# Performance work log

Hardware: AMD Instinct MI355X
Metric: run time of the kernel (lower is better)

The kernel has to match this reference:

```python
import jax, jax.numpy as jnp
import numpy as np

VOCAB = 30000  # opts.numofingr
EPS = 1e-12


def setup_inputs() -> dict:
    key = jax.random.key(0)
    ks = jax.random.split(key, 8)
    B, L = 4096, 20
    ingrs = jax.random.randint(ks[0], (B, L), 0, VOCAB, dtype=jnp.int32)
    lengths = jax.random.randint(ks[1], (B,), 0, 21, dtype=jnp.int32)
    # MLP params: Linear(VOCAB,512) -> ReLU -> Linear(512,1024) -> ReLU -> Linear(1024,2047)
    # Stored so that one-hot @ W1 == W1[ingr]; i.e. W1 has shape [VOCAB, 512].
    W1 = jax.random.normal(ks[2], (VOCAB, 512), dtype=jnp.float32) * (1.0 / np.sqrt(VOCAB))
    b1 = jax.random.normal(ks[3], (512,), dtype=jnp.float32) * 0.01
    W2 = jax.random.normal(ks[4], (512, 1024), dtype=jnp.float32) * (1.0 / np.sqrt(512))
    b2 = jax.random.normal(ks[5], (1024,), dtype=jnp.float32) * 0.01
    W3 = jax.random.normal(ks[6], (1024, 2047), dtype=jnp.float32) * (1.0 / np.sqrt(1024))
    b3 = jax.random.normal(ks[7], (2047,), dtype=jnp.float32) * 0.01
    return {"ingrs": ingrs, "lengths": lengths,
            "W1": W1, "b1": b1, "W2": W2, "b2": b2, "W3": W3, "b3": b3}


def reference(ingrs, lengths, W1, b1, W2, b2, W3, b3):
    # One-hot x MLP first layer == embedding row gather: [B, L, 512]
    h1 = jax.nn.relu(W1[ingrs] + b1)
    h2 = jax.nn.relu(jnp.einsum('blh,hk->blk', h1, W2) + b2)   # [B, L, 1024]
    emb = jnp.einsum('blk,ko->blo', h2, W3) + b3               # [B, L, 2047]
    # L2-normalize each ingredient embedding (torch norm(p=2, dim=1) on [1,2047])
    nrm = jnp.sqrt(jnp.sum(emb * emb, axis=-1, keepdims=True))
    emb = emb / jnp.maximum(nrm, EPS)
    # Masked sum over valid ingredients (ingr_ln truncation in the source)
    L = ingrs.shape[1]
    mask = (jnp.arange(L)[None, :] < lengths[:, None]).astype(emb.dtype)  # [B, L]
    return jnp.einsum('blo,bl->bo', emb, mask)                 # [B, 2047]
```

## Files before the change

kernel.cpp:

```cpp
#include <hip/hip_runtime.h>

#define VOCAB 30000
#define MPAD  30080
#define MT_PAD 240

typedef __attribute__((ext_vector_type(8))) short bf16x8;
typedef __attribute__((ext_vector_type(4))) float f32x4;

__device__ __forceinline__ unsigned short f2bf(float f) {
    unsigned int u = __builtin_bit_cast(unsigned int, f);
    u += 0x7fffu + ((u >> 16) & 1u);
    return (unsigned short)(u >> 16);
}
__device__ __forceinline__ float bf2f(unsigned int h) {
    unsigned int u = h << 16;
    return __builtin_bit_cast(float, u);
}

__device__ __forceinline__ void async16(const void* g, void* l) {
    __builtin_amdgcn_global_load_lds(
        (__attribute__((address_space(1))) void*)g,
        (__attribute__((address_space(3))) void*)l, 16, 0, 0);
}

__global__ void k_mark(const int* __restrict__ ingrs, const int* __restrict__ lengths,
                       int* __restrict__ flags, int* __restrict__ cnt)
{
    const int i = blockIdx.x * 256 + threadIdx.x;
    if (i == 0) *cnt = 0;
    if (i >= 4096 * 20) return;
    const int b = i / 20;
    const int l = i - b * 20;
    if (l < lengths[b]) flags[ingrs[i]] = 1;
}

__global__ void k_assign(const int* __restrict__ flags, int* __restrict__ remap,
                         int* __restrict__ cnt)
{
    const int i = blockIdx.x * 256 + threadIdx.x;
    if (i < VOCAB && flags[i] == 1) remap[i] = atomicAdd(cnt, 1);
}


__device__ __forceinline__ void transpose_body(
    const float* __restrict__ in, unsigned short* __restrict__ out,
    int K, int Nin, int n0, int k0, int tid, float (*t)[65])
{
#pragma unroll
    for (int p = 0; p < 16; ++p) {
        const int lin = p * 256 + tid;
        const int kk = lin >> 6, nn = lin & 63;
        const int n = n0 + nn;
        t[kk][nn] = (n < Nin) ? in[(size_t)(k0 + kk) * Nin + n] : 0.f;
    }
    __syncthreads();
#pragma unroll
    for (int p = 0; p < 16; ++p) {
        const int lin = p * 256 + tid;
        const int nn = lin >> 6, kk = lin & 63;
        out[(size_t)(n0 + nn) * K + k0 + kk] = f2bf(t[kk][nn]);
    }
}

__device__ __forceinline__ void gemm_body(
    unsigned short* smem,
    const unsigned short* __restrict__ A, const unsigned short* __restrict__ BT,
    const float* __restrict__ bias, int bias_n, unsigned short* __restrict__ C,
    int K, int N, int relu, int mc, int id, int nt_shift)
{
    const int w  = id >> 3;
    const int n_tile = w & ((1 << nt_shift) - 1);
    const int m_tile = (id & 7) + ((w >> nt_shift) << 3);
    const int m0 = m_tile * 128;
    if (m0 >= mc) return;
    const int n0 = n_tile * 128;

    unsigned short* As = smem;
    unsigned short* Bs = smem + 8192;

    const int tid  = threadIdx.x;
    const int lane = tid & 63;
    const int wid  = tid >> 6;
    const int wr   = wid >> 1;
    const int wc   = wid & 1;
    const int q  = lane >> 4;
    const int ml = lane & 15;

    f32x4 acc[4][4];
    const f32x4 zero = {0.f, 0.f, 0.f, 0.f};
#pragma unroll
    for (int i = 0; i < 4; ++i)
#pragma unroll
        for (int j = 0; j < 4; ++j) acc[i][j] = zero;

    const int rg = lane >> 3;
    const int kc = (lane & 7) ^ rg;
    const unsigned short* pA = A  + (size_t)(m0 + wid * 32 + rg) * K + kc * 8;
    const unsigned short* pB = BT + (size_t)(n0 + wid * 32 + rg) * K + kc * 8;
    unsigned short* lA = &As[wid * 4 * 512 + lane * 8];
    unsigned short* lB = &Bs[wid * 4 * 512 + lane * 8];

    const int swz0 = (q ^ (ml & 7)) * 8;

    for (int k0 = 0; k0 < K; k0 += 64) {
#pragma unroll
        for (int gg = 0; gg < 4; ++gg) {
            async16(pA + (size_t)gg * 8 * K, lA + gg * 512);
            async16(pB + (size_t)gg * 8 * K, lB + gg * 512);
        }
        pA += 64; pB += 64;
        __syncthreads();

        bf16x8 af[4], bfr[4];
#pragma unroll
        for (int t = 0; t < 4; ++t) {
            af[t]  = *(const bf16x8*)&As[(wr * 64 + t * 16 + ml) * 64 + swz0];
            bfr[t] = *(const bf16x8*)&Bs[(wc * 64 + t * 16 + ml) * 64 + swz0];
        }
#pragma unroll
        for (int i = 0; i < 4; ++i)
#pragma unroll
            for (int j = 0; j < 4; ++j)
                acc[i][j] = __builtin_amdgcn_mfma_f32_16x16x32_bf16(
                    af[i], bfr[j], acc[i][j], 0, 0, 0);
#pragma unroll
        for (int t = 0; t < 4; ++t) {
            af[t]  = *(const bf16x8*)&As[(wr * 64 + t * 16 + ml) * 64 + (swz0 ^ 32)];
            bfr[t] = *(const bf16x8*)&Bs[(wc * 64 + t * 16 + ml) * 64 + (swz0 ^ 32)];
        }
#pragma unroll
        for (int i = 0; i < 4; ++i)
#pragma unroll
            for (int j = 0; j < 4; ++j)
                acc[i][j] = __builtin_amdgcn_mfma_f32_16x16x32_bf16(
                    af[i], bfr[j], acc[i][j], 0, 0, 0);

        __syncthreads();
    }

#pragma unroll
    for (int i = 0; i < 4; ++i) {
#pragma unroll
        for (int j = 0; j < 4; ++j) {
#pragma unroll
            for (int r = 0; r < 4; ++r) {
                const int rl = wr * 64 + i * 16 + q * 4 + r;
                const int cl = wc * 64 + j * 16 + ml;
                float v = acc[i][j][r];
                const int col = n0 + cl;
                v += (col < bias_n) ? bias[col] : 0.f;
                if (relu) v = fmaxf(v, 0.f);
                smem[rl * 136 + cl] = f2bf(v);
            }
        }
    }
    __syncthreads();
#pragma unroll
    for (int p = 0; p < 8; ++p) {
        const int rr = p * 16 + (tid >> 4);
        const int cc = tid & 15;
        const uint4 val = *(const uint4*)&smem[rr * 136 + cc * 8];
        *(uint4*)&C[(size_t)(m0 + rr) * N + n0 + cc * 8] = val;
    }
}

__global__ __launch_bounds__(256)
void k_prep(const float* __restrict__ W1, const float* __restrict__ b1,
            const int* __restrict__ flags, const int* __restrict__ remap,
            unsigned short* __restrict__ A1,
            const float* __restrict__ W2, unsigned short* __restrict__ W2T)
{
    __shared__ float t[64][65];
    const int bid = blockIdx.x;
    const int tid = threadIdx.x;

    if (bid < 15000) {
        const int id = bid * 2 + (tid >> 7);
        if (flags[id] != 1) return;
        const int row = remap[id];
        const int k4  = (tid & 127) * 4;
        const float4 w  = *(const float4*)(W1 + (size_t)id * 512 + k4);
        const float4 bb = *(const float4*)(b1 + k4);
        unsigned short o[4];
        o[0] = f2bf(fmaxf(w.x + bb.x, 0.f));
        o[1] = f2bf(fmaxf(w.y + bb.y, 0.f));
        o[2] = f2bf(fmaxf(w.z + bb.z, 0.f));
        o[3] = f2bf(fmaxf(w.w + bb.w, 0.f));
        *(uint2*)(A1 + (size_t)row * 512 + k4) = *(const uint2*)o;
    } else {
        const int local = bid - 15000;
        transpose_body(W2, W2T, 512, 1024, (local & 15) * 64, (local >> 4) * 64, tid, t);
    }
}

__global__ __launch_bounds__(256)
void k_gemm1(const unsigned short* __restrict__ A1, const unsigned short* __restrict__ W2T,
             const float* __restrict__ b2, unsigned short* __restrict__ H2,
             const int* __restrict__ cnt,
             const float* __restrict__ W3, unsigned short* __restrict__ W3T,
             const int* __restrict__ ingrs, const int* __restrict__ lengths,
             const int* __restrict__ remap, int* __restrict__ slots)
{
    __shared__ __align__(16) unsigned short smem[128 * 136];
    const int bid = blockIdx.x;
    if (bid < MT_PAD * 8) {
        const int mc = (*cnt + 127) & ~127;
        gemm_body(smem, A1, W2T, b2, 1024, H2, 512, 1024, 1, mc, bid, 3);
    } else if (bid < MT_PAD * 8 + 512) {
        const int local = bid - MT_PAD * 8;
        transpose_body(W3, W3T, 1024, 2047, (local & 31) * 64, (local >> 5) * 64,
                       threadIdx.x, (float(*)[65])smem);
    } else {
        const int i = (bid - (MT_PAD * 8 + 512)) * 256 + threadIdx.x;
        if (i < 4096 * 20) {
            const int b = i / 20;
            const int l = i - b * 20;
            if (l < lengths[b]) slots[i] = remap[ingrs[i]];
        }
    }
}

#define G2_NK 16
#define G2_K  1024
#define G2_N  2048
#define G2_MT 120

#define MF(a, b, c) __builtin_amdgcn_mfma_f32_16x16x32_bf16(a, b, c, 0, 0, 0)

__global__ __launch_bounds__(512, 2)
void k_gemm2(const unsigned short* __restrict__ A, const unsigned short* __restrict__ BT,
             const float* __restrict__ bias, unsigned short* __restrict__ C,
             const int* __restrict__ cnt)
{
    __shared__ __align__(16) unsigned short lds[65536];

    const int id = blockIdx.x;
    const int w  = id >> 3;
    const int n_tile = w & 7;
    const int m_tile = (id & 7) + ((w >> 3) << 3);
    const int m0 = m_tile * 256;
    const int mc = (*cnt + 255) & ~255;
    if (m0 >= mc) return;
    const int n0 = n_tile * 256;

    const int tid  = threadIdx.x;
    const int lane = tid & 63;
    const int w0   = tid >> 6;
    const int wr   = w0 >> 2;
    const int wc   = w0 & 3;
    const int q    = lane >> 4;
    const int ml   = lane & 15;
    const int m7   = ml & 7;

    f32x4 acc[8][4];
    const f32x4 zero = {0.f, 0.f, 0.f, 0.f};
#pragma unroll
    for (int i = 0; i < 8; ++i)
#pragma unroll
        for (int j = 0; j < 4; ++j) acc[i][j] = zero;

    const int rg = lane >> 3;
    const int kc = (lane & 7) ^ rg;
    const unsigned short* pA0 = A  + (size_t)(m0 + w0 * 32 + rg) * G2_K + kc * 8;
    const unsigned short* pB0 = BT + (size_t)(n0 + w0 * 32 + rg) * G2_K + kc * 8;
    const int dstoff = w0 * 2048 + lane * 8;

#define G2_STAGE(BUF, KT) do {                                             \
        const unsigned short* _sa = pA0 + (size_t)(KT) * 64;               \
        const unsigned short* _sb = pB0 + (size_t)(KT) * 64;               \
        unsigned short* _da = &lds[(BUF) * 16384 + dstoff];                \
        unsigned short* _db = &lds[32768 + (BUF) * 16384 + dstoff];        \
        _Pragma("unroll")                                                  \
        for (int g = 0; g < 4; ++g) {                                      \
            async16(_sa + (size_t)g * 8 * G2_K, _da + g * 512);            \
            async16(_sb + (size_t)g * 8 * G2_K, _db + g * 512);            \
        }                                                                  \
    } while (0)

#define LDA(I, S) (*(const bf16x8*)&lds[cb + ((wr * 128 + (I) * 16 + ml) * 64) + ((((S) * 4 + q) ^ m7) * 8)])
#define LDB(J, S) (*(const bf16x8*)&lds[32768 + cb + ((wc * 64 + (J) * 16 + ml) * 64) + ((((S) * 4 + q) ^ m7) * 8)])

#define G2_PHASE(I0) do {                                                  \
        bf16x8 a00 = LDA(I0, 0), a01 = LDA(I0, 1);                         \
        bf16x8 a10 = LDA(I0 + 1, 0), a11 = LDA(I0 + 1, 1);                 \
        __builtin_amdgcn_s_barrier();                                      \
        asm volatile("s_waitcnt lgkmcnt(0)" ::: "memory");                 \
        __builtin_amdgcn_sched_barrier(0);                                 \
        __builtin_amdgcn_s_setprio(1);                                     \
        _Pragma("unroll")                                                  \
        for (int j = 0; j < 4; ++j) acc[I0][j]     = MF(a00, bfr[0][j], acc[I0][j]);     \
        _Pragma("unroll")                                                  \
        for (int j = 0; j < 4; ++j) acc[I0 + 1][j] = MF(a10, bfr[0][j], acc[I0 + 1][j]); \
        _Pragma("unroll")                                                  \
        for (int j = 0; j < 4; ++j) acc[I0][j]     = MF(a01, bfr[1][j], acc[I0][j]);     \
        _Pragma("unroll")                                                  \
        for (int j = 0; j < 4; ++j) acc[I0 + 1][j] = MF(a11, bfr[1][j], acc[I0 + 1][j]); \
        __builtin_amdgcn_s_setprio(0);                                     \
        __builtin_amdgcn_s_barrier();                                      \
    } while (0)

    G2_STAGE(0, 0);
    G2_STAGE(1, 1);
    asm volatile("s_waitcnt vmcnt(8)" ::: "memory");
    __builtin_amdgcn_s_barrier();

    for (int t = 0; t < G2_NK; ++t) {
        const int cb = (t & 1) * 16384;

        bf16x8 bfr[2][4];
#pragma unroll
        for (int s = 0; s < 2; ++s)
#pragma unroll
            for (int j = 0; j < 4; ++j) bfr[s][j] = LDB(j, s);

        G2_PHASE(0);
        G2_PHASE(2);
        G2_PHASE(4);
        G2_PHASE(6);

        if (t + 2 < G2_NK) {
            G2_STAGE(t & 1, t + 2);
            asm volatile("s_waitcnt vmcnt(8)" ::: "memory");
        } else {
            asm volatile("s_waitcnt vmcnt(0)" ::: "memory");
        }
        __builtin_amdgcn_s_barrier();
    }

#undef G2_PHASE
#undef LDA
#undef LDB
#undef G2_STAGE

    float bv[4];
#pragma unroll
    for (int j = 0; j < 4; ++j) {
        const int col = n0 + wc * 64 + j * 16 + ml;
        bv[j] = (col < 2047) ? bias[col] : 0.f;
    }
    for (int h = 0; h < 2; ++h) {
        if (wr == h) {
#pragma unroll
            for (int i = 0; i < 8; ++i)
#pragma unroll
                for (int j = 0; j < 4; ++j)
#pragma unroll
                    for (int r = 0; r < 4; ++r) {
                        const float v = acc[i][j][r] + bv[j];
                        lds[(i * 16 + q * 4 + r) * 280 + wc * 64 + j * 16 + ml] = f2bf(v);
                    }
        }
        __syncthreads();
#pragma unroll
        for (int p = 0; p < 8; ++p) {
            const int row  = p * 16 + (tid >> 5);
            const int c8   = (tid & 31) * 8;
            const int grow = m0 + h * 128 + row;
            if (grow < MPAD) {
                *(uint4*)&C[(size_t)grow * G2_N + n0 + c8] =
                    *(const uint4*)&lds[row * 280 + c8];
            }
        }
        __syncthreads();
    }
}

__global__ __launch_bounds__(64)
void k_gather(const int* __restrict__ lengths, const int* __restrict__ slots,
              const unsigned short* __restrict__ Table, float* __restrict__ out)
{
    const int b    = blockIdx.x;
    const int lane = threadIdx.x;

    float acc[32];
#pragma unroll
    for (int j = 0; j < 32; ++j) acc[j] = 0.f;

    const int len = lengths[b];
    if (len > 0) {
        uint4 u[4];
        {
            const int slot = slots[b * 20];
            const uint4* rp = (const uint4*)(Table + (size_t)slot * 2048);
#pragma unroll
            for (int c = 0; c < 4; ++c) u[c] = rp[c * 64 + lane];
        }
        for (int l = 0; l < len; ++l) {
            uint4 cu[4];
#pragma unroll
            for (int c = 0; c < 4; ++c) cu[c] = u[c];
            if (l + 1 < len) {
                const int ns = slots[b * 20 + l + 1];
                const uint4* rp = (const uint4*)(Table + (size_t)ns * 2048);
#pragma unroll
                for (int c = 0; c < 4; ++c) u[c] = rp[c * 64 + lane];
            }
            float v[32];
#pragma unroll
            for (int c = 0; c < 4; ++c) {
                v[c*8+0] = bf2f(cu[c].x & 0xffffu); v[c*8+1] = bf2f(cu[c].x >> 16);
                v[c*8+2] = bf2f(cu[c].y & 0xffffu); v[c*8+3] = bf2f(cu[c].y >> 16);
                v[c*8+4] = bf2f(cu[c].z & 0xffffu); v[c*8+5] = bf2f(cu[c].z >> 16);
                v[c*8+6] = bf2f(cu[c].w & 0xffffu); v[c*8+7] = bf2f(cu[c].w >> 16);
            }
            float s = 0.f;
#pragma unroll
            for (int j = 0; j < 32; ++j) s += v[j] * v[j];
#pragma unroll
            for (int off = 1; off < 64; off <<= 1) s += __shfl_xor(s, off, 64);
            const float invn = 1.0f / fmaxf(sqrtf(s), 1e-12f);
#pragma unroll
            for (int j = 0; j < 32; ++j) acc[j] += v[j] * invn;
        }
    }

    const size_t base = (size_t)b * 2047;
#pragma unroll
    for (int c = 0; c < 4; ++c) {
        const int col = (c * 64 + lane) * 8;
#pragma unroll
        for (int j = 0; j < 8; ++j)
            if (col + j < 2047) out[base + col + j] = acc[c * 8 + j];
    }
}


extern "C" void kernel_launch(void* const* d_in, const int* in_sizes, int n_in,
                              void* d_out, int out_size, void* d_ws, size_t ws_size,
                              hipStream_t stream)
{
    const int*   ingrs   = (const int*)d_in[0];
    const int*   lengths = (const int*)d_in[1];
    const float* W1 = (const float*)d_in[2];
    const float* b1 = (const float*)d_in[3];
    const float* W2 = (const float*)d_in[4];
    const float* b2 = (const float*)d_in[5];
    const float* W3 = (const float*)d_in[6];
    const float* b3 = (const float*)d_in[7];
    float* out = (float*)d_out;

    char* ws = (char*)d_ws;
    unsigned short* A1    = (unsigned short*)(ws);
    unsigned short* H2    = (unsigned short*)(ws + 30801920);
    unsigned short* Table = (unsigned short*)(ws + 92405760);
    unsigned short* W2T   = (unsigned short*)(ws + 215613440);
    unsigned short* W3T   = (unsigned short*)(ws + 216662016);
    int*            flags = (int*)(ws + 220856320);
    int*            remap = (int*)(ws + 220976320);
    int*            cnt   = (int*)(ws + 221096320);
    int*            slots = (int*)(ws + 221216448);

    k_mark  <<<(4096 * 20 + 255) / 256, 256, 0, stream>>>(ingrs, lengths, flags, cnt);
    k_assign<<<(VOCAB + 255) / 256, 256, 0, stream>>>(flags, remap, cnt);
    k_prep<<<15128, 256, 0, stream>>>(W1, b1, flags, remap, A1, W2, W2T);
    k_gemm1<<<MT_PAD * 8 + 512 + 320, 256, 0, stream>>>(
        A1, W2T, b2, H2, cnt, W3, W3T, ingrs, lengths, remap, slots);
    k_gemm2<<<G2_MT * 8, 512, 0, stream>>>(H2, W3T, b3, Table, cnt);

    k_gather<<<4096, 64, 0, stream>>>(lengths, slots, Table, out);
}
```

Baseline: 320.5 us.

## Split GEMM tile loads into half-tile units interleaved with MFMA phases

The GEMM main loop is restructured so global-to-LDS async loads are issued as half-tile units (top/bottom 128 rows of A and B), and those units are interleaved across four MFMA phases instead of being issued all at once after compute. The phases now work on 4x4 MFMA blocks per K-slice rather than 2 rows across both slices. The aim is to spread memory traffic through the compute and keep the prefetch pipeline fuller. This adds finer-grained buffer-hazard reasoning: the next-buffer loads for the second half are issued while the current buffer is still being read, which risks races if the barrier ordering is wrong.

```diff
diff --git a/kernel.cpp b/kernel.cpp
--- a/kernel.cpp
+++ b/kernel.cpp
@@ -261,76 +261,91 @@
 
     const int rg = lane >> 3;
     const int kc = (lane & 7) ^ rg;
-    const unsigned short* pA0 = A  + (size_t)(m0 + w0 * 32 + rg) * G2_K + kc * 8;
-    const unsigned short* pB0 = BT + (size_t)(n0 + w0 * 32 + rg) * G2_K + kc * 8;
-    const int dstoff = w0 * 2048 + lane * 8;
-
-#define G2_STAGE(BUF, KT) do {                                             \
-        const unsigned short* _sa = pA0 + (size_t)(KT) * 64;               \
-        const unsigned short* _sb = pB0 + (size_t)(KT) * 64;               \
-        unsigned short* _da = &lds[(BUF) * 16384 + dstoff];                \
-        unsigned short* _db = &lds[32768 + (BUF) * 16384 + dstoff];        \
-        _Pragma("unroll")                                                  \
-        for (int g = 0; g < 4; ++g) {                                      \
-            async16(_sa + (size_t)g * 8 * G2_K, _da + g * 512);            \
-            async16(_sb + (size_t)g * 8 * G2_K, _db + g * 512);            \
-        }                                                                  \
+    const unsigned short* gA = A  + (size_t)(m0 + w0 * 16 + rg) * G2_K + kc * 8;
+    const unsigned short* gB = BT + (size_t)(n0 + w0 * 16 + rg) * G2_K + kc * 8;
+    const int dst0 = (w0 * 16) * 64 + lane * 8;
+
+#define G2_U(AB, H, B_, T) do {                                                \
+        const unsigned short* _s = ((AB) ? gB : gA)                            \
+            + (size_t)((H) * 128) * G2_K + (size_t)(T) * 64;                   \
+        unsigned short* _d = &lds[(AB) * 32768 + (B_) * 16384                  \
+            + ((H) * 128) * 64 + dst0];                                        \
+        async16(_s, _d);                                                       \
+        async16(_s + (size_t)8 * G2_K, _d + 8 * 64);                           \
     } while (0)
 
 #define LDA(I, S) (*(const bf16x8*)&lds[cb + ((wr * 128 + (I) * 16 + ml) * 64) + ((((S) * 4 + q) ^ m7) * 8)])
 #define LDB(J, S) (*(const bf16x8*)&lds[32768 + cb + ((wc * 64 + (J) * 16 + ml) * 64) + ((((S) * 4 + q) ^ m7) * 8)])
 
-#define G2_PHASE(I0) do {                                                  \
-        bf16x8 a00 = LDA(I0, 0), a01 = LDA(I0, 1);                         \
-        bf16x8 a10 = LDA(I0 + 1, 0), a11 = LDA(I0 + 1, 1);                 \
-        __builtin_amdgcn_s_barrier();                                      \
-        asm volatile("s_waitcnt lgkmcnt(0)" ::: "memory");                 \
-        __builtin_amdgcn_sched_barrier(0);                                 \
-        __builtin_amdgcn_s_setprio(1);                                     \
-        _Pragma("unroll")                                                  \
-        for (int j = 0; j < 4; ++j) acc[I0][j]     = MF(a00, bfr[0][j], acc[I0][j]);     \
-        _Pragma("unroll")                                                  \
-        for (int j = 0; j < 4; ++j) acc[I0 + 1][j] = MF(a10, bfr[0][j], acc[I0 + 1][j]); \
-        _Pragma("unroll")                                                  \
-        for (int j = 0; j < 4; ++j) acc[I0][j]     = MF(a01, bfr[1][j], acc[I0][j]);     \
-        _Pragma("unroll")                                                  \
-        for (int j = 0; j < 4; ++j) acc[I0 + 1][j] = MF(a11, bfr[1][j], acc[I0 + 1][j]); \
-        __builtin_amdgcn_s_setprio(0);                                     \
-        __builtin_amdgcn_s_barrier();                                      \
-    } while (0)
-
-    G2_STAGE(0, 0);
-    G2_STAGE(1, 1);
-    asm volatile("s_waitcnt vmcnt(8)" ::: "memory");
-    __builtin_amdgcn_s_barrier();
+#define G2_MFMA16(AI0, BF)                                                     \
+        _Pragma("unroll")                                                      \
+        for (int i = 0; i < 4; ++i)                                            \
+        _Pragma("unroll")                                                      \
+        for (int j = 0; j < 4; ++j)                                            \
+            acc[(AI0) + i][j] = MF(afr[i], BF[j], acc[(AI0) + i][j]);
+
+#define G2_BAR()  __builtin_amdgcn_s_barrier()
+#define G2_LGKM() do { asm volatile("s_waitcnt lgkmcnt(0)" ::: "memory");      \
+                       __builtin_amdgcn_sched_barrier(0); } while (0)
+
+    G2_U(0, 0, 0, 0); G2_U(0, 1, 0, 0); G2_U(1, 0, 0, 0); G2_U(1, 1, 0, 0);
+    G2_U(0, 0, 1, 1); G2_U(1, 0, 1, 1);
+    asm volatile("s_waitcnt vmcnt(4)" ::: "memory");
+    G2_BAR();
 
     for (int t = 0; t < G2_NK; ++t) {
-        const int cb = (t & 1) * 16384;
-
-        bf16x8 bfr[2][4];
-#pragma unroll
-        for (int s = 0; s < 2; ++s)
-#pragma unroll
-            for (int j = 0; j < 4; ++j) bfr[s][j] = LDB(j, s);
-
-        G2_PHASE(0);
-        G2_PHASE(2);
-        G2_PHASE(4);
-        G2_PHASE(6);
-
-        if (t + 2 < G2_NK) {
-            G2_STAGE(t & 1, t + 2);
-            asm volatile("s_waitcnt vmcnt(8)" ::: "memory");
-        } else {
-            asm volatile("s_waitcnt vmcnt(0)" ::: "memory");
-        }
-        __builtin_amdgcn_s_barrier();
-    }
-
-#undef G2_PHASE
+        const int cb  = (t & 1) * 16384;
+        const int cur = t & 1, nxt = cur ^ 1;
+        bf16x8 afr[4], bS0[4], bS1[4];
+
+#pragma unroll
+        for (int j = 0; j < 4; ++j) bS0[j] = LDB(j, 0);
+#pragma unroll
+        for (int i = 0; i < 4; ++i) afr[i] = LDA(i, 0);
+        if (t + 1 < G2_NK) G2_U(0, 1, nxt, t + 1);
+        G2_BAR(); G2_LGKM();
+        __builtin_amdgcn_s_setprio(1);
+        G2_MFMA16(0, bS0)
+        __builtin_amdgcn_s_setprio(0);
+        G2_BAR();
+
+#pragma unroll
+        for (int i = 0; i < 4; ++i) afr[i] = LDA(4 + i, 0);
+        if (t + 1 < G2_NK) G2_U(1, 1, nxt, t + 1);
+        G2_BAR(); G2_LGKM();
+        __builtin_amdgcn_s_setprio(1);
+        G2_MFMA16(4, bS0)
+        __builtin_amdgcn_s_setprio(0);
+        G2_BAR();
+
+#pragma unroll
+        for (int j = 0; j < 4; ++j) bS1[j] = LDB(j, 1);
+#pragma unroll
+        for (int i = 0; i < 4; ++i) afr[i] = LDA(i, 1);
+        G2_BAR(); G2_LGKM();
+        __builtin_amdgcn_s_setprio(1);
+        G2_MFMA16(0, bS1)
+        __builtin_amdgcn_s_setprio(0);
+        G2_BAR();
+
+#pragma unroll
+        for (int i = 0; i < 4; ++i) afr[i] = LDA(4 + i, 1);
+        if (t + 2 < G2_NK) { G2_U(0, 0, cur, t + 2); G2_U(1, 0, cur, t + 2); }
+        G2_BAR(); G2_LGKM();
+        __builtin_amdgcn_s_setprio(1);
+        G2_MFMA16(4, bS1)
+        __builtin_amdgcn_s_setprio(0);
+        if (t + 2 < G2_NK) asm volatile("s_waitcnt vmcnt(4)" ::: "memory");
+        else               asm volatile("s_waitcnt vmcnt(0)" ::: "memory");
+        G2_BAR();
+    }
+
+#undef G2_U
 #undef LDA
 #undef LDB
-#undef G2_STAGE
+#undef G2_MFMA16
+#undef G2_BAR
+#undef G2_LGKM
 
     float bv[4];
 #pragma unroll
```

Measured after the change: 311.2 us. 2.9% less time.
